# Optimization experiments

Measured on AMD Instinct MI355X. Metric: run time of the kernel, lower is better.

Reference implementation:

```python
import jax, jax.numpy as jnp
import numpy as np

B, C_LIDAR, C_CAM = 2, 384, 80
H = W = 180
HW = H * W
HID, NCLS, P, NH, DFF, L, NMS_K = 128, 10, 200, 8, 256, 2, 3


def conv2d(x, w, b):
    y = jax.lax.conv_general_dilated(x, w, (1, 1), 'SAME', dimension_numbers=('NCHW', 'OIHW', 'NCHW'))
    return y + b[None, :, None, None]


def conv1d3(x, w, b):
    y = jax.lax.conv_general_dilated(x, w, (1,), 'SAME', dimension_numbers=('NCH', 'OIH', 'NCH'))
    return y + b[None, :, None]


def layer_norm(x, g, b, eps=1e-5):
    mu = jnp.mean(x, -1, keepdims=True)
    var = jnp.mean((x - mu) ** 2, -1, keepdims=True)
    return (x - mu) * jax.lax.rsqrt(var + eps) * g + b


def mha(q, k, v, wqkv, bqkv, wo, bo):
    Bq, Nq, C = q.shape
    dh = C // NH
    qh = (q @ wqkv[0].T + bqkv[0]).reshape(Bq, Nq, NH, dh)
    kh = (k @ wqkv[1].T + bqkv[1]).reshape(k.shape[0], -1, NH, dh)
    vh = (v @ wqkv[2].T + bqkv[2]).reshape(v.shape[0], -1, NH, dh)
    att = jax.nn.softmax(jnp.einsum('bqhd,bkhd->bhqk', qh, kh) * np.float32(1.0 / np.sqrt(dh)), axis=-1)
    out = jnp.einsum('bhqk,bkhd->bqhd', att, vh).reshape(Bq, Nq, C)
    return out @ wo.T + bo


def posembed(pos, w1, b1, g, bt, w2, b2):
    # Conv1d(2->C,k1) + BN(inference) + ReLU + Conv1d(C->C,k1); pos [B,N,2] -> [B,N,C]
    x = pos @ w1.T + b1
    x = jax.nn.relu(x * g + bt)
    return x @ w2.T + b2


def reference(lidar, cam, shared_w, shared_b, fused_w, fused_b, hm_w1, hm_b1, hm_g, hm_beta, hm_w2, hm_b2, ce_w, ce_b, pe_w1, pe_b1, pe_g, pe_beta, pe_w2, pe_b2, attn_wqkv, attn_bqkv, attn_wo, attn_bo, ln_g, ln_b, ffn_w1, ffn_b1, ffn_w2, ffn_b2, hc_w1, hc_b1, hc_g, hc_beta, hc_w2, hc_b2, hh_w1, hh_b1, hh_g, hh_beta, hh_w2, hh_b2):
    cam_feat = conv2d(cam, fused_w, fused_b)            # [B,HID,H,W]
    lidar_feat = conv2d(lidar, shared_w, shared_b)      # [B,HID,H,W]
    lidar_flat = lidar_feat.reshape(B, HID, HW)
    key_flat = cam_feat.reshape(B, HID, HW).transpose(0, 2, 1)   # [B,HW,HID]
    # heatmap head: ConvModule(conv+BN+ReLU) then conv -> classes
    h = jax.nn.relu(conv2d(lidar_feat, hm_w1, hm_b1) * hm_g[None, :, None, None] + hm_beta[None, :, None, None])
    dense_heatmap = conv2d(h, hm_w2, hm_b2)             # [B,NCLS,H,W]
    heatmap = jax.nn.sigmoid(jax.lax.stop_gradient(dense_heatmap))
    # max-pool local-max NMS
    pad = NMS_K // 2
    inner = jax.lax.reduce_window(heatmap, -jnp.inf, jax.lax.max, (1, 1, NMS_K, NMS_K), (1, 1, 1, 1), 'VALID')
    local_max = jnp.zeros_like(heatmap).at[:, :, pad:-pad, pad:-pad].set(inner)
    # nuScenes: classes 8,9 use kernel-size-1 pooling (identity)
    local_max = local_max.at[:, 8].set(heatmap[:, 8]).at[:, 9].set(heatmap[:, 9])
    heatmap = heatmap * (heatmap == local_max)
    # top-k proposals over flattened class*HW scores (== descending argsort[:P])
    _, top = jax.lax.top_k(heatmap.reshape(B, -1), P)
    top_cls = top // HW
    top_idx = top % HW
    qf = jnp.take_along_axis(lidar_flat, top_idx[:, None, :], axis=2)   # [B,HID,P]
    one_hot = jax.nn.one_hot(top_cls, NCLS, dtype=qf.dtype)             # [B,P,NCLS]
    qf = qf + (one_hot @ ce_w.T + ce_b).transpose(0, 2, 1)
    # BEV position grid (x/y cell centers, ij order matching HW flattening)
    gx = jnp.arange(H, dtype=qf.dtype) + 0.5
    gy = jnp.arange(W, dtype=qf.dtype) + 0.5
    bev = jnp.stack(jnp.meshgrid(gx, gy, indexing='ij'), -1).reshape(HW, 2)
    qpos = bev[top_idx]                                  # [B,P,2]
    x = qf.transpose(0, 2, 1)                            # [B,P,HID]
    for i in range(L):
        qpe = posembed(qpos, pe_w1[i, 0], pe_b1[i, 0], pe_g[i, 0], pe_beta[i, 0], pe_w2[i, 0], pe_b2[i, 0])
        kpe = posembed(bev[None], pe_w1[i, 1], pe_b1[i, 1], pe_g[i, 1], pe_beta[i, 1], pe_w2[i, 1], pe_b2[i, 1])
        k = key_flat + kpe
        sa = mha(x + qpe, x + qpe, x + qpe, attn_wqkv[i, 0], attn_bqkv[i, 0], attn_wo[i, 0], attn_bo[i, 0])
        x = layer_norm(x + sa, ln_g[i, 0], ln_b[i, 0])
        ca = mha(x + qpe, k, k, attn_wqkv[i, 1], attn_bqkv[i, 1], attn_wo[i, 1], attn_bo[i, 1])
        x = layer_norm(x + ca, ln_g[i, 1], ln_b[i, 1])
        f = jax.nn.relu(x @ ffn_w1[i].T + ffn_b1[i]) @ ffn_w2[i].T + ffn_b2[i]
        x = layer_norm(x + f, ln_g[i, 2], ln_b[i, 2])
        xc = x.transpose(0, 2, 1)                        # [B,HID,P]
        yc = jax.nn.relu(conv1d3(xc, hc_w1[i], hc_b1[i]) * hc_g[i][None, :, None] + hc_beta[i][None, :, None])
        center = conv1d3(yc, hc_w2[i], hc_b2[i]) + qpos.transpose(0, 2, 1)
        yh = jax.nn.relu(conv1d3(xc, hh_w1[i], hh_b1[i]) * hh_g[i][None, :, None] + hh_beta[i][None, :, None])
        hm_pred = conv1d3(yh, hh_w2[i], hh_b2[i])
        qpos = jax.lax.stop_gradient(center).transpose(0, 2, 1)   # .detach().clone().permute
    return jnp.concatenate([center, hm_pred], axis=1)   # [B, 2+NCLS, P]


def _n(key, i, shape, s=0.02):
    return s * jax.random.normal(jax.random.fold_in(key, i), shape, dtype=jnp.float32)


def setup_inputs():
    key = jax.random.key(0)
    z, o = jnp.zeros, jnp.ones
    return dict(
        lidar=jax.random.normal(jax.random.fold_in(key, 100), (B, C_LIDAR, H, W), dtype=jnp.float32),
        cam=jax.random.normal(jax.random.fold_in(key, 101), (B, C_CAM, H, W), dtype=jnp.float32),
        shared_w=_n(key, 0, (HID, C_LIDAR, 3, 3)), shared_b=z((HID,)),
        fused_w=_n(key, 1, (HID, C_CAM, 3, 3)), fused_b=z((HID,)),
        hm_w1=_n(key, 2, (HID, HID, 3, 3)), hm_b1=z((HID,)), hm_g=o((HID,)), hm_beta=z((HID,)),
        hm_w2=_n(key, 3, (NCLS, HID, 3, 3)), hm_b2=z((NCLS,)),
        ce_w=_n(key, 4, (HID, NCLS)), ce_b=z((HID,)),
        pe_w1=_n(key, 5, (L, 2, HID, 2), 0.1), pe_b1=z((L, 2, HID)),
        pe_g=o((L, 2, HID)), pe_beta=z((L, 2, HID)),
        pe_w2=_n(key, 6, (L, 2, HID, HID)), pe_b2=z((L, 2, HID)),
        attn_wqkv=_n(key, 7, (L, 2, 3, HID, HID), 0.05), attn_bqkv=z((L, 2, 3, HID)),
        attn_wo=_n(key, 8, (L, 2, HID, HID), 0.05), attn_bo=z((L, 2, HID)),
        ln_g=o((L, 3, HID)), ln_b=z((L, 3, HID)),
        ffn_w1=_n(key, 9, (L, DFF, HID)), ffn_b1=z((L, DFF)),
        ffn_w2=_n(key, 10, (L, HID, DFF)), ffn_b2=z((L, HID)),
        hc_w1=_n(key, 11, (L, HID, HID, 3)), hc_b1=z((L, HID)), hc_g=o((L, HID)), hc_beta=z((L, HID)),
        hc_w2=_n(key, 12, (L, 2, HID, 3)), hc_b2=z((L, 2)),
        hh_w1=_n(key, 13, (L, HID, HID, 3)), hh_b1=z((L, HID)), hh_g=o((L, HID)), hh_beta=z((L, HID)),
        hh_w2=_n(key, 14, (L, NCLS, HID, 3)), hh_b2=z((L, NCLS)),
    )
```

## Files before the change

### kernel.cpp

```cpp
#include <hip/hip_runtime.h>
#include <hip/hip_bf16.h>

typedef __hip_bfloat16 bf16;
typedef _Float16 f16;

#define HW 32400
#define NCLS 10
#define PQ 200
#define HIDDEN 128
#define NSPLIT 45
#define SPLITLEN 720
#define CHK 32
#define CAP 6144
#define NBIN 4096
#define L2E 1.44269504f

typedef __attribute__((ext_vector_type(8))) _Float16 half8;
typedef __attribute__((ext_vector_type(8))) short short8;
typedef __attribute__((ext_vector_type(4))) short short4v;
typedef __attribute__((ext_vector_type(4))) float f32x4;

__device__ __forceinline__ float b2f(bf16 v) { return __bfloat162float(v); }
__device__ __forceinline__ void stf(float* p, float v) { *p = v; }
__device__ __forceinline__ void stf(bf16* p, float v) { *p = __float2bfloat16(v); }
__device__ __forceinline__ float ldsel(const void* p, long i, unsigned isbf) {
  return isbf ? __bfloat162float(((const bf16*)p)[i]) : ((const float*)p)[i];
}
__device__ __forceinline__ float ldf(const float* p, long i) { return p[i]; }
__device__ __forceinline__ float ldf(const bf16* p, long i) { return __bfloat162float(p[i]); }
__device__ __forceinline__ short f2bf_bits(float v) {
  union { bf16 h; short s; } u; u.h = __float2bfloat16(v); return u.s;
}
__device__ __forceinline__ short f2h_bits(float v) {
  union { f16 h; short s; } u; u.h = (f16)v; return u.s;
}

__global__ void detect_k(const unsigned* __restrict__ L, unsigned* __restrict__ FLAGS)
{
  __shared__ unsigned cnt[2];
  int tid = threadIdx.x;
  if (tid < 2) cnt[tid] = 0;
  __syncthreads();
  unsigned nz = 0, pl = 0;
  for (int w = tid; w < 4096; w += 256) {
    unsigned u = L[w];
    if (u) {
      nz++;
      unsigned e = (u >> 7) & 0xFF;
      if (e >= 110 && e <= 140) pl++;
    }
  }
  atomicAdd(&cnt[0], nz);
  atomicAdd(&cnt[1], pl);
  __syncthreads();
  if (tid == 0) {
    FLAGS[0] = (2u * cnt[1] > cnt[0]) ? 1u : 0u;
    FLAGS[1] = 0u;
  }
}

struct CvtArgs { const void* src[40]; int n[40]; int off[40]; };
__global__ __launch_bounds__(256) void cvt_k(CvtArgs a, float* __restrict__ dst,
                                             const unsigned* __restrict__ FLAGS)
{
  int j = blockIdx.y;
  unsigned isbf = FLAGS[0];
  int n = a.n[j];
  const void* s = a.src[j];
  float* d = dst + a.off[j];
  for (int t = blockIdx.x * 256 + threadIdx.x; t < n; t += gridDim.x * 256)
    d[t] = ldsel(s, t, isbf);
}

__global__ __launch_bounds__(256) void wprep_k(const float* __restrict__ Wsrc,
    short* __restrict__ WB, int N, int K, int KB, int NTG, int split,
    const unsigned* __restrict__ FLAGS, int dynmode)
{
  unsigned isbf = dynmode ? FLAGS[0] : 0u;
  long total = (long)(split ? 2 : 1) * 9 * KB * NTG * 512;
  for (long t = (long)blockIdx.x * 256 + threadIdx.x; t < total;
       t += (long)gridDim.x * 256) {
    long r = t;
    int k = (int)(r & 31); r >>= 5;
    int n16 = (int)(r & 15); r >>= 4;
    int nt = (int)(r % NTG); r /= NTG;
    int kb = (int)(r % KB); r /= KB;
    int tap = (int)(r % 9); r /= 9;
    int plane = (int)r;
    int n = nt * 16 + n16, kk = kb * 32 + k;
    float v = 0.f;
    if (n < N && kk < K) v = Wsrc[((long)n * K + kk) * 9 + tap];
    short outv;
    if (isbf) {
      outv = (plane == 0) ? f2bf_bits(v) : (short)0;
    } else {
      f16 h = (f16)v;
      if (plane == 0) outv = f2h_bits((float)h);
      else outv = f2h_bits((v - (float)h) * 4096.0f);
    }
    WB[t] = outv;
  }
}

template <int MODE, int WM, int WN, int MT, int NT, int CW, typename CT>
__global__ __launch_bounds__(256) void conv_mfma(
    const void* __restrict__ A, const unsigned* __restrict__ FLAGS, int dyn,
    int gate, long abatch,
    const short* __restrict__ WB, const float* __restrict__ bias,
    const float* __restrict__ g, const float* __restrict__ beta, int act,
    CT* __restrict__ C, long cbatch, int N, int K, int KB, int NTG)
{
  constexpr int CPR = 180 / CW;
  constexpr int TOT = 180 * CPR;
  constexpr int BAND = (TOT + 7) / 8;
  constexpr int PXS = WM * MT * 16 + 2;
  constexpr int AW = 3 * PXS * 40;
  __shared__ __align__(16) short Ah[AW];
  __shared__ __align__(16) short Al[MODE == 3 ? AW : 8];
  if (gate >= 0 && FLAGS[0] != (unsigned)gate) return;
  int gsw = blockIdx.x;
  int idx = (gsw & 7) * BAND + (gsw >> 3);
  if (idx >= TOT) return;
  unsigned isbf = dyn ? FLAGS[0] : 0u;
  int bz = blockIdx.z;
  int y = idx / CPR;
  int x0 = (idx % CPR) * CW;
  int tid = threadIdx.x;
  int w = tid >> 6, lane = tid & 63;
  int lane15 = lane & 15, lgrp = lane >> 4;
  int wm = w % WM, wn = w / WM;
  int mbase = wm * MT * 16;
  int nbase = wn * NT * 16;
  f32x4 accM[MT][NT] = {};
  f32x4 accC[MODE == 3 ? MT : 1][MODE == 3 ? NT : 1] = {};
  long planeStride = (long)9 * KB * NTG * 512;

  for (int kb = 0; kb < KB; kb++) {
    __syncthreads();
    for (int u = tid; u < 3 * PXS * 4; u += 256) {
      int px = u % PXS;
      int t2 = u / PXS;
      int kg = t2 & 3, row = t2 >> 2;
      int gx = x0 + px - 1, gy = y + row - 1;
      bool in = (gx >= 0 && gx < 180 && gy >= 0 && gy < 180);
      long gbase = (long)bz * abatch + (long)(kb * 32 + kg * 8) * HW +
                   (long)gy * 180 + gx;
      short8 hv, lv;
#pragma unroll
      for (int j = 0; j < 8; j++) {
        int kk = kb * 32 + kg * 8 + j;
        if constexpr (MODE == 1) {
          hv[j] = (in && kk < K) ? ((const short*)A)[gbase + (long)j * HW]
                                 : (short)0;
        } else {
          float v = (in && kk < K) ? ldsel(A, gbase + (long)j * HW, isbf) : 0.f;
          f16 h = (f16)v;
          hv[j] = f2h_bits((float)h);
          if constexpr (MODE == 3) lv[j] = f2h_bits((v - (float)h) * 4096.0f);
        }
      }
      int o = (row * PXS + px) * 40 + kg * 8;
      *(short8*)&Ah[o] = hv;
      if constexpr (MODE == 3) *(short8*)&Al[o] = lv;
    }
    __syncthreads();
#pragma unroll
    for (int tap = 0; tap < 9; tap++) {
      int ty = tap / 3, tx = tap % 3;
      const short* wb = WB + (((long)tap * KB + kb) * NTG) * 512;
      if constexpr (MODE == 1) {
        short8 bh[NT];
#pragma unroll
        for (int nt = 0; nt < NT; nt++) {
          long o = (long)(wn * NT + nt) * 512 + lane15 * 32 + lgrp * 8;
          bh[nt] = *(const short8*)(wb + o);
        }
        short8 ah[MT];
#pragma unroll
        for (int mt = 0; mt < MT; mt++) {
          int px = mbase + mt * 16 + lane15 + tx;
          ah[mt] = *(const short8*)&Ah[(ty * PXS + px) * 40 + lgrp * 8];
        }
#pragma unroll
        for (int mt = 0; mt < MT; mt++)
#pragma unroll
          for (int nt = 0; nt < NT; nt++)
            accM[mt][nt] = __builtin_amdgcn_mfma_f32_16x16x32_bf16(
                ah[mt], bh[nt], accM[mt][nt], 0, 0, 0);
      } else {
        half8 bh[NT], bl[MODE == 3 ? NT : 1];
#pragma unroll
        for (int nt = 0; nt < NT; nt++) {
          long o = (long)(wn * NT + nt) * 512 + lane15 * 32 + lgrp * 8;
          bh[nt] = *(const half8*)(wb + o);
          if constexpr (MODE == 3) bl[nt] = *(const half8*)(wb + planeStride + o);
        }
        half8 ah[MT], al[MODE == 3 ? MT : 1];
#pragma unroll
        for (int mt = 0; mt < MT; mt++) {
          int px = mbase + mt * 16 + lane15 + tx;
          int o = (ty * PXS + px) * 40 + lgrp * 8;
          ah[mt] = *(const half8*)&Ah[o];
          if constexpr (MODE == 3) al[mt] = *(const half8*)&Al[o];
        }
#pragma unroll
        for (int mt = 0; mt < MT; mt++)
#pragma unroll
          for (int nt = 0; nt < NT; nt++) {
            accM[mt][nt] = __builtin_amdgcn_mfma_f32_16x16x32_f16(
                ah[mt], bh[nt], accM[mt][nt], 0, 0, 0);
            if constexpr (MODE == 3) {
              accC[mt][nt] = __builtin_amdgcn_mfma_f32_16x16x32_f16(
                  al[mt], bh[nt], accC[mt][nt], 0, 0, 0);
              accC[mt][nt] = __builtin_amdgcn_mfma_f32_16x16x32_f16(
                  ah[mt], bl[nt], accC[mt][nt], 0, 0, 0);
            }
          }
      }
    }
  }
  int pixbase = y * 180 + x0;
#pragma unroll
  for (int mt = 0; mt < MT; mt++) {
    int m = mbase + mt * 16 + lgrp * 4;
    if (m >= CW) continue;
#pragma unroll
    for (int nt = 0; nt < NT; nt++) {
      int n = nbase + nt * 16 + lane15;
      if (n >= N) continue;
      float bi = bias[n];
      float gg = g ? g[n] : 1.f;
      float bb = g ? beta[n] : 0.f;
      long base = (long)bz * cbatch + (long)n * HW + pixbase + m;
      float vv[4];
#pragma unroll
      for (int r = 0; r < 4; r++) {
        float v = accM[mt][nt][r];
        if constexpr (MODE == 3) v += accC[mt][nt][r] * (1.f / 4096.f);
        v += bi;
        if (g) v = v * gg + bb;
        if (act == 1) v = fmaxf(v, 0.f);
        else if (act == 2) v = 1.f / (1.f + expf(-v));
        vv[r] = v;
      }
      if constexpr (sizeof(CT) == 4) {
        if (m + 3 < CW) {
          f32x4 ov; ov[0] = vv[0]; ov[1] = vv[1]; ov[2] = vv[2]; ov[3] = vv[3];
          *(f32x4*)&C[base] = ov;
        } else {
#pragma unroll
          for (int r = 0; r < 4; r++) if (m + r < CW) C[base + r] = vv[r];
        }
      } else {
        if (m + 3 < CW) {
          short4v ov;
#pragma unroll
          for (int r = 0; r < 4; r++) ov[r] = f2bf_bits(vv[r]);
          *(short4v*)&C[base] = ov;
        } else {
#pragma unroll
          for (int r = 0; r < 4; r++)
            if (m + r < CW) *((short*)&C[base + r]) = f2bf_bits(vv[r]);
        }
      }
    }
  }
}

__global__ __launch_bounds__(256) void kvproj_k(
    const bf16* __restrict__ A1, const bf16* __restrict__ A2,
    const float* __restrict__ Wf, const float* __restrict__ bias,
    bf16* __restrict__ C)
{
  __shared__ __align__(16) short As[64 * 40];
  int m0 = blockIdx.x * 64;
  int n0 = blockIdx.y * 64;
  int b = blockIdx.z;
  int tid = threadIdx.x;
  int w = tid >> 6, lane = tid & 63;
  int lane15 = lane & 15, lgrp = lane >> 4;
  int wm = w & 1, wn = w >> 1;
  const bf16* A1b = A1 + (long)b * 128 * HW;
  f32x4 acc[2][2] = {};
  for (int kb = 0; kb < 4; kb++) {
    __syncthreads();
    for (int e = tid; e < 2048; e += 256) {
      int k = e >> 6, m = e & 63;
      int gm = m0 + m;
      float v = 0.f;
      if (gm < HW) {
        long idx = (long)(kb * 32 + k) * HW + gm;
        v = b2f(A1b[idx]) + b2f(A2[idx]);
      }
      As[m * 40 + k] = f2bf_bits(v);
    }
    __syncthreads();
    short8 bh[2];
#pragma unroll
    for (int nt = 0; nt < 2; nt++) {
      int n = n0 + wn * 32 + nt * 16 + lane15;
      const float* wr = Wf + (long)n * 128 + kb * 32 + lgrp * 8;
      float4 w0 = *(const float4*)wr;
      float4 w1 = *(const float4*)(wr + 4);
      short8 t;
      t[0] = f2bf_bits(w0.x); t[1] = f2bf_bits(w0.y);
      t[2] = f2bf_bits(w0.z); t[3] = f2bf_bits(w0.w);
      t[4] = f2bf_bits(w1.x); t[5] = f2bf_bits(w1.y);
      t[6] = f2bf_bits(w1.z); t[7] = f2bf_bits(w1.w);
      bh[nt] = t;
    }
    short8 ah[2];
#pragma unroll
    for (int mt = 0; mt < 2; mt++) {
      int m = wm * 32 + mt * 16 + lane15;
      ah[mt] = *(const short8*)&As[m * 40 + lgrp * 8];
    }
#pragma unroll
    for (int mt = 0; mt < 2; mt++)
#pragma unroll
      for (int nt = 0; nt < 2; nt++)
        acc[mt][nt] = __builtin_amdgcn_mfma_f32_16x16x32_bf16(
            ah[mt], bh[nt], acc[mt][nt], 0, 0, 0);
  }
#pragma unroll
  for (int mt = 0; mt < 2; mt++) {
    int mq = m0 + wm * 32 + mt * 16 + lgrp * 4;
    if (mq >= HW) continue;
#pragma unroll
    for (int nt = 0; nt < 2; nt++) {
      int n = n0 + wn * 32 + nt * 16 + lane15;
      float bi = bias[n];
      short4v ov;
#pragma unroll
      for (int r = 0; r < 4; r++) ov[r] = f2bf_bits(acc[mt][nt][r] + bi);
      *(short4v*)&C[(long)b * 256 * HW + (long)n * HW + mq] = ov;
    }
  }
}

template <typename AT, typename CT>
__global__ __launch_bounds__(256) void gemm_k(
    const AT* __restrict__ A, const AT* __restrict__ A2, int lda, int amode,
    long abatch,
    const float* __restrict__ W, const float* __restrict__ bias, int act,
    const float* __restrict__ res,
    const float* __restrict__ pe1w, const float* __restrict__ pe1b,
    const float* __restrict__ pe1g, const float* __restrict__ pe1bt,
    CT* __restrict__ C, int ldc, int cmode, long cbatch,
    int M, int N, int K)
{
  __shared__ __align__(16) float As[16][68];
  __shared__ __align__(16) float Ws[16][68];
  int b = blockIdx.z;
  int m0 = blockIdx.x * 64, n0 = blockIdx.y * 64;
  int tid = threadIdx.x;
  int nt = tid & 15, mt = tid >> 4;
  float acc[4][4] = {};
  const AT* Ab = A + (long)b * abatch;
  for (int k0 = 0; k0 < K; k0 += 16) {
    if (amode == 0) {
      for (int e = tid; e < 1024; e += 256) {
        int m = e >> 4, k = e & 15;
        float v = 0.f;
        if (m0 + m < M) {
          long idx = (long)(m0 + m) * lda + k0 + k;
          v = ldf(Ab, idx);
          if (A2) v += ldf(A2, idx);
        }
        As[k][m] = v;
      }
    } else if (amode == 2) {
      for (int e = tid; e < 1024; e += 256) {
        int m = e & 63, k = e >> 6;
        float v = 0.f;
        int gm = m0 + m;
        if (gm < M) {
          float p0 = (float)(gm / 180) + 0.5f;
          float p1 = (float)(gm % 180) + 0.5f;
          int kk = k0 + k;
          float t = p0 * pe1w[kk * 2] + p1 * pe1w[kk * 2 + 1] + pe1b[kk];
          t = t * pe1g[kk] + pe1bt[kk];
          v = fmaxf(t, 0.f);
        }
        As[k][m] = v;
      }
    } else {
      const float* qp = (const float*)A;
      for (int e = tid; e < 1024; e += 256) {
        int m = e & 63, k = e >> 6;
        float v = 0.f;
        int gm = m0 + m;
        if (gm < M) {
          float p0 = qp[gm * 2], p1 = qp[gm * 2 + 1];
          int kk = k0 + k;
          float t = p0 * pe1w[kk * 2] + p1 * pe1w[kk * 2 + 1] + pe1b[kk];
          t = t * pe1g[kk] + pe1bt[kk];
          v = fmaxf(t, 0.f);
        }
        As[k][m] = v;
      }
    }
    for (int e = tid; e < 1024; e += 256) {
      int n = e >> 4, k = e & 15;
      float v = 0.f;
      if (n0 + n < N) v = W[(long)(n0 + n) * K + k0 + k];
      Ws[k][n] = v;
    }
    __syncthreads();
#pragma unroll
    for (int kk = 0; kk < 16; kk++) {
      float4 av = *(const float4*)&As[kk][mt * 4];
      float4 wv = *(const float4*)&Ws[kk][nt * 4];
      float am[4] = {av.x, av.y, av.z, av.w};
      float wn[4] = {wv.x, wv.y, wv.z, wv.w};
#pragma unroll
      for (int mi = 0; mi < 4; mi++)
#pragma unroll
        for (int ni = 0; ni < 4; ni++)
          acc[mi][ni] = fmaf(am[mi], wn[ni], acc[mi][ni]);
    }
    __syncthreads();
  }
#pragma unroll
  for (int mi = 0; mi < 4; mi++) {
    int m = m0 + mt * 4 + mi;
    if (m >= M) continue;
#pragma unroll
    for (int ni = 0; ni < 4; ni++) {
      int n = n0 + nt * 4 + ni;
      if (n >= N) continue;
      float v = acc[mi][ni];
      if (bias) v += bias[n];
      if (act == 1) v = fmaxf(v, 0.f);
      if (res) v += res[(long)m * ldc + n];
      long ci = (cmode == 0) ? ((long)b * cbatch + (long)m * ldc + n)
                             : ((long)b * cbatch + (long)n * ldc + m);
      stf(&C[ci], v);
    }
  }
}

__global__ void nms_k(const float* __restrict__ HEAT, float* __restrict__ SCORE)
{
  int t = blockIdx.x * 256 + threadIdx.x;
  if (t >= 2 * NCLS * HW) return;
  int b = t / (NCLS * HW); int r = t % (NCLS * HW);
  int cls = r / HW; int n = r % HW;
  const float* hb = HEAT + ((long)(b * NCLS + cls)) * HW;
  float v = hb[n];
  bool keep = true;
  if (cls < 8) {
    int y = n / 180, x = n % 180;
    if (y == 0 || y == 179 || x == 0 || x == 179) keep = false;
    else {
      float mx = -1e30f;
#pragma unroll
      for (int dy = -1; dy <= 1; dy++)
#pragma unroll
        for (int dx = -1; dx <= 1; dx++)
          mx = fmaxf(mx, hb[(y + dy) * 180 + x + dx]);
      keep = (v == mx);
    }
  }
  SCORE[(long)b * (NCLS * HW) + r] = keep ? v : 0.f;
}

__global__ void zero_u32(unsigned* p, int n)
{
  int t = blockIdx.x * 256 + threadIdx.x;
  if (t < n) p[t] = 0;
}

__global__ __launch_bounds__(256) void hist_k(const float* __restrict__ SCORE,
                                              unsigned* __restrict__ HIST)
{
  __shared__ unsigned lh[NBIN];
  int b = blockIdx.y;
  for (int e = threadIdx.x; e < NBIN; e += 256) lh[e] = 0;
  __syncthreads();
  int start = blockIdx.x * 1350;
  const float* sb = SCORE + (long)b * (NCLS * HW);
  for (int e = start + threadIdx.x; e < start + 1350; e += 256) {
    unsigned bits = __float_as_uint(sb[e]);
    atomicAdd(&lh[bits >> 18], 1u);
  }
  __syncthreads();
  for (int e = threadIdx.x; e < NBIN; e += 256) {
    unsigned c = lh[e];
    if (c) atomicAdd(&HIST[b * NBIN + e], c);
  }
}

__global__ void thresh_k(const unsigned* __restrict__ HIST, unsigned* __restrict__ THR)
{
  __shared__ unsigned ps[256];
  int b = blockIdx.x;
  const unsigned* hb = HIST + b * NBIN;
  unsigned s = 0;
  for (int j = 0; j < 16; j++) s += hb[threadIdx.x * 16 + j];
  ps[threadIdx.x] = s;
  __syncthreads();
  if (threadIdx.x == 0) {
    unsigned cum = 0; int t = 255;
    for (; t > 0; t--) { if (cum + ps[t] >= PQ) break; cum += ps[t]; }
    int bin = t * 16 + 15;
    for (; bin > t * 16; bin--) { unsigned c = hb[bin]; if (cum + c >= PQ) break; cum += c; }
    if (bin < 1) bin = 1;
    THR[b] = (unsigned)bin;
  }
}

__global__ void collect_k(const float* __restrict__ SCORE, const unsigned* __restrict__ THR,
                          unsigned* __restrict__ ACNT, unsigned long long* __restrict__ CAND)
{
  int t = blockIdx.x * 256 + threadIdx.x;
  if (t >= 2 * NCLS * HW) return;
  int b = t / (NCLS * HW); int r = t % (NCLS * HW);
  float v = SCORE[(long)b * (NCLS * HW) + r];
  unsigned bits = __float_as_uint(v);
  if ((bits >> 18) >= THR[b]) {
    unsigned slot = atomicAdd(&ACNT[b], 1u);
    if (slot < CAP) CAND[(long)b * CAP + slot] =
        ((unsigned long long)bits << 32) | (unsigned)(~r);
  }
}

__global__ __launch_bounds__(64) void select_k(
    const unsigned long long* __restrict__ CAND, const unsigned* __restrict__ ACNT,
    unsigned* __restrict__ TOPC, unsigned* __restrict__ TOPI, float* __restrict__ QPA)
{
  __shared__ unsigned long long cnd[CAP];
  int b = blockIdx.x;
  int lane = threadIdx.x;
  unsigned cnt = ACNT[b]; if (cnt > CAP) cnt = CAP;
  for (int e = lane; e < (int)cnt; e += 64) cnd[e] = CAND[(long)b * CAP + e];
  __syncthreads();
  for (int p = 0; p < PQ; p++) {
    unsigned long long best = 0;
    for (int e = lane; e < (int)cnt; e += 64) { unsigned long long c = cnd[e]; if (c > best) best = c; }
#pragma unroll
    for (int o = 32; o; o >>= 1) {
      unsigned long long other = __shfl_xor(best, o, 64);
      if (other > best) best = other;
    }
    for (int e = lane; e < (int)cnt; e += 64) if (best != 0 && cnd[e] == best) cnd[e] = 0;
    if (lane == 0) {
      unsigned idx = (best == 0) ? 0u : ~(unsigned)(best & 0xFFFFFFFFull);
      if (idx >= NCLS * HW) idx = 0;
      unsigned cls = idx / HW, n = idx % HW;
      TOPC[b * PQ + p] = cls; TOPI[b * PQ + p] = n;
      QPA[((long)(b * PQ + p)) * 2 + 0] = (float)(n / 180) + 0.5f;
      QPA[((long)(b * PQ + p)) * 2 + 1] = (float)(n % 180) + 0.5f;
    }
    __syncthreads();
  }
}

__global__ void gather_k(const float* __restrict__ LIDF, const unsigned* __restrict__ TOPC,
                         const unsigned* __restrict__ TOPI, const float* __restrict__ cew,
                         const float* __restrict__ ceb, float* __restrict__ X)
{
  int t = blockIdx.x * 256 + threadIdx.x;
  if (t >= 2 * PQ * HIDDEN) return;
  int c = t & 127; int r = t >> 7; int p = r % PQ; int b = r / PQ;
  unsigned n = TOPI[b * PQ + p]; unsigned cls = TOPC[b * PQ + p];
  if (n >= HW) n = 0;
  if (cls >= NCLS) cls = 0;
  X[t] = LIDF[((long)(b * HIDDEN + c)) * HW + n] + cew[c * NCLS + cls] + ceb[c];
}

__global__ __launch_bounds__(64) void self_attn_k(const float* __restrict__ SQKV,
                                                  float* __restrict__ SAO)
{
  int q = blockIdx.x, h = blockIdx.y, b = blockIdx.z;
  int lane = threadIdx.x;
  const float* qp = SQKV + ((long)(b * PQ + q)) * 384 + h * 16;
  float qv[16];
#pragma unroll
  for (int d = 0; d < 16; d++) qv[d] = qp[d] * 0.25f;
  float sv[4]; int kks[4]; int nk = 0;
  float lmax = -1e30f;
  for (int kk = lane; kk < PQ; kk += 64) {
    const float* kp = SQKV + ((long)(b * PQ + kk)) * 384 + 128 + h * 16;
    float s = 0.f;
#pragma unroll
    for (int d = 0; d < 16; d++) s = fmaf(qv[d], kp[d], s);
    sv[nk] = s; kks[nk] = kk; nk++;
    lmax = fmaxf(lmax, s);
  }
#pragma unroll
  for (int o = 32; o; o >>= 1) lmax = fmaxf(lmax, __shfl_xor(lmax, o, 64));
  float lsum = 0.f; float acc[16] = {};
  for (int t = 0; t < nk; t++) {
    float p = expf(sv[t] - lmax);
    lsum += p;
    const float* vp = SQKV + ((long)(b * PQ + kks[t])) * 384 + 256 + h * 16;
#pragma unroll
    for (int d = 0; d < 16; d++) acc[d] = fmaf(p, vp[d], acc[d]);
  }
#pragma unroll
  for (int o = 32; o; o >>= 1) lsum += __shfl_xor(lsum, o, 64);
#pragma unroll
  for (int d = 0; d < 16; d++) {
    float v = acc[d];
#pragma unroll
    for (int o = 32; o; o >>= 1) v += __shfl_xor(v, o, 64);
    if (lane == 0) SAO[((long)(b * PQ + q)) * HIDDEN + h * 16 + d] = v / lsum;
  }
}

__global__ __launch_bounds__(256) void flash_mfma_k(const float* __restrict__ QH,
                                                    const bf16* __restrict__ KVT,
                                                    float* __restrict__ PART)
{
  __shared__ __align__(16) short Qs[64 * 40];
  __shared__ __align__(16) short Ks[2][32 * 40];
  __shared__ __align__(16) short Vs[2][16 * 40];
  __shared__ __align__(16) short Ps[4][16 * 40];
  int s = blockIdx.x, h = blockIdx.y;
  int b = blockIdx.z >> 2, qb = blockIdx.z & 3;
  int tid = threadIdx.x;
  int w = tid >> 6, lane = tid & 63;
  int lane15 = lane & 15, lgrp = lane >> 4;
  const short* Kb = (const short*)KVT + ((long)b * 256 + h * 16) * HW;
  const short* Vb = Kb + (long)128 * HW;
  int nbeg = s * SPLITLEN;

  for (int e = tid; e < 2 * 32 * 16; e += 256) {
    int buf = e >> 9, rr = e & 511;
    int kk = rr >> 4, d2 = rr & 15;
    Ks[buf][kk * 40 + 16 + d2] = 0;
  }
  {
    int q = tid >> 2, dg = tid & 3;
    int gq = qb * 64 + q;
    short8 v = {};
    if (dg < 2 && gq < PQ) {
      const float* qp = QH + ((long)(b * PQ + gq)) * HIDDEN + h * 16 + dg * 8;
#pragma unroll
      for (int j = 0; j < 8; j++) v[j] = f2bf_bits(qp[j] * 0.25f);
    }
    *(short8*)&Qs[q * 40 + dg * 8] = v;
  }

  auto stageKV = [&](int t, int buf) {
    int kb0 = nbeg + t * CHK;
    for (int e = tid; e < 512; e += 256) {
      int d = e >> 5, kk = e & 31;
      long gk = kb0 + kk; if (gk >= HW) gk = HW - 1;
      long go = (long)d * HW + gk;
      Ks[buf][kk * 40 + d] = Kb[go];
      Vs[buf][d * 40 + kk] = Vb[go];
    }
  };

  stageKV(0, 0);
  __syncthreads();

  short8 aq = *(const short8*)&Qs[(w * 16 + lane15) * 40 + lgrp * 8];
  float m[4] = {-1e30f, -1e30f, -1e30f, -1e30f};
  float l[4] = {0.f, 0.f, 0.f, 0.f};
  f32x4 accO = {};
  const int NTL = (SPLITLEN + CHK - 1) / CHK;
  for (int t = 0; t < NTL; t++) {
    int cur = t & 1;
    if (t + 1 < NTL) stageKV(t + 1, cur ^ 1);
    int valid = SPLITLEN - t * CHK; if (valid > CHK) valid = CHK;
    short8 bk0 = *(const short8*)&Ks[cur][lane15 * 40 + lgrp * 8];
    short8 bk1 = *(const short8*)&Ks[cur][(16 + lane15) * 40 + lgrp * 8];
    f32x4 z = {};
    f32x4 s0 = __builtin_amdgcn_mfma_f32_16x16x32_bf16(aq, bk0, z, 0, 0, 0);
    f32x4 s1 = __builtin_amdgcn_mfma_f32_16x16x32_bf16(aq, bk1, z, 0, 0, 0);
    bool msk0 = (lane15 >= valid);
    bool msk1 = (16 + lane15 >= valid);
#pragma unroll
    for (int r = 0; r < 4; r++) {
      float x0 = msk0 ? -1e30f : s0[r];
      float x1 = msk1 ? -1e30f : s1[r];
      float mx = fmaxf(x0, x1);
      mx = fmaxf(mx, __shfl_xor(mx, 1, 64));
      mx = fmaxf(mx, __shfl_xor(mx, 2, 64));
      mx = fmaxf(mx, __shfl_xor(mx, 4, 64));
      mx = fmaxf(mx, __shfl_xor(mx, 8, 64));
      float mn = fmaxf(m[r], mx);
      float p0 = exp2f((x0 - mn) * L2E);
      float p1 = exp2f((x1 - mn) * L2E);
      float sum = p0 + p1;
      sum += __shfl_xor(sum, 1, 64);
      sum += __shfl_xor(sum, 2, 64);
      sum += __shfl_xor(sum, 4, 64);
      sum += __shfl_xor(sum, 8, 64);
      float al = exp2f((m[r] - mn) * L2E);
      l[r] = l[r] * al + sum;
      m[r] = mn;
      accO[r] *= al;
      Ps[w][(lgrp * 4 + r) * 40 + lane15] = f2bf_bits(p0);
      Ps[w][(lgrp * 4 + r) * 40 + 16 + lane15] = f2bf_bits(p1);
    }
    short8 ap = *(const short8*)&Ps[w][lane15 * 40 + lgrp * 8];
    short8 bv = *(const short8*)&Vs[cur][lane15 * 40 + lgrp * 8];
    accO = __builtin_amdgcn_mfma_f32_16x16x32_bf16(ap, bv, accO, 0, 0, 0);
    __syncthreads();
  }
  long base = ((((long)(b * 8 + h)) * NSPLIT + s) * PQ) * 18;
#pragma unroll
  for (int r = 0; r < 4; r++) {
    int gq = qb * 64 + w * 16 + lgrp * 4 + r;
    if (gq < PQ) {
      long ro = base + (long)gq * 18;
      PART[ro + lane15] = accO[r];
      if (lane15 == 0) { PART[ro + 16] = m[r]; PART[ro + 17] = l[r]; }
    }
  }
}

__global__ void combine_k(const float* __restrict__ PART, float* __restrict__ CAO)
{
  int t = blockIdx.x * 256 + threadIdx.x;
  if (t >= 2 * 8 * PQ * 16) return;
  int d = t & 15; int r = t >> 4;
  int q = r % PQ; r /= PQ;
  int h = r & 7; int b = r >> 3;
  long base = (((long)(b * 8 + h)) * NSPLIT) * PQ * 18 + (long)q * 18;
  float M = -1e30f;
  for (int s = 0; s < NSPLIT; s++) M = fmaxf(M, PART[base + (long)s * PQ * 18 + 16]);
  float L = 0.f, O = 0.f;
  for (int s = 0; s < NSPLIT; s++) {
    long p0 = base + (long)s * PQ * 18;
    float w = expf(PART[p0 + 16] - M);
    L += PART[p0 + 17] * w;
    O += PART[p0 + d] * w;
  }
  CAO[((long)(b * PQ + q)) * HIDDEN + h * 16 + d] = (L > 0.f) ? O / L : 0.f;
}

__global__ __launch_bounds__(256) void ln_k(const float* __restrict__ PRE,
                                            const float* __restrict__ g,
                                            const float* __restrict__ bta,
                                            float* __restrict__ X)
{
  int row = blockIdx.x * 4 + (threadIdx.x >> 6);
  int lane = threadIdx.x & 63;
  const float* p = PRE + (long)row * HIDDEN;
  float v0 = p[lane], v1 = p[lane + 64];
  float s = v0 + v1;
#pragma unroll
  for (int o = 32; o; o >>= 1) s += __shfl_xor(s, o, 64);
  float mu = s * (1.f / 128.f);
  float d0 = v0 - mu, d1 = v1 - mu;
  float vs = d0 * d0 + d1 * d1;
#pragma unroll
  for (int o = 32; o; o >>= 1) vs += __shfl_xor(vs, o, 64);
  float rs = rsqrtf(vs * (1.f / 128.f) + 1e-5f);
  float* xo = X + (long)row * HIDDEN;
  xo[lane] = d0 * rs * g[lane] + bta[lane];
  xo[lane + 64] = d1 * rs * g[lane + 64] + bta[lane + 64];
}

__global__ __launch_bounds__(128) void conv1d_k(const float* __restrict__ X,
                                                const float* __restrict__ w,
                                                const float* __restrict__ bias,
                                                const float* __restrict__ g,
                                                const float* __restrict__ beta,
                                                float* __restrict__ Y)
{
  int p = blockIdx.x, b = blockIdx.y;
  int co = threadIdx.x;
  __shared__ float xs[3][HIDDEN];
  for (int e = co; e < 3 * HIDDEN; e += HIDDEN) {
    int t = e >> 7, c = e & 127;
    int pp = p + t - 1;
    xs[t][c] = (pp >= 0 && pp < PQ) ? X[((long)(b * PQ + pp)) * HIDDEN + c] : 0.f;
  }
  __syncthreads();
  const float* wr = w + (long)co * HIDDEN * 3;
  float acc = 0.f;
  for (int c = 0; c < HIDDEN; c++) {
    acc = fmaf(xs[0][c], wr[c * 3 + 0], acc);
    acc = fmaf(xs[1][c], wr[c * 3 + 1], acc);
    acc = fmaf(xs[2][c], wr[c * 3 + 2], acc);
  }
  float v = (acc + bias[co]) * g[co] + beta[co];
  Y[((long)(b * PQ + p)) * HIDDEN + co] = fmaxf(v, 0.f);
}

__global__ void head2_k(const float* __restrict__ Y, const float* __restrict__ w,
                        const float* __restrict__ bias, const float* __restrict__ qpos,
                        float* __restrict__ OUT, int N, float* __restrict__ qnext)
{
  int t = blockIdx.x * 256 + threadIdx.x;
  if (t >= 2 * N * PQ) return;
  int p = t % PQ; int r = t / PQ; int co = r % N; int b = r / N;
  const float* wr = w + (long)co * HIDDEN * 3;
  float acc = 0.f;
  for (int tap = 0; tap < 3; tap++) {
    int pp = p + tap - 1;
    if (pp < 0 || pp >= PQ) continue;
    const float* yr = Y + ((long)(b * PQ + pp)) * HIDDEN;
    for (int c = 0; c < HIDDEN; c++)
      acc = fmaf(yr[c], wr[c * 3 + tap], acc);
  }
  float v = acc + bias[co];
  if (qpos) v += qpos[((long)(b * PQ + p)) * 2 + co];
  OUT[((long)(b * N + co)) * PQ + p] = v;
  if (qnext) qnext[((long)(b * PQ + p)) * 2 + co] = v;
}

__global__ void out_k(const float* __restrict__ CENT, const float* __restrict__ HMP,
                      void* __restrict__ out, const unsigned* __restrict__ FLAGS)
{
  int t = blockIdx.x * 256 + threadIdx.x;
  if (t >= 2 * 12 * PQ) return;
  int p = t % PQ; int r = t / PQ; int ch = r % 12; int b = r / 12;
  float v = (ch < 2) ? CENT[((long)(b * 2 + ch)) * PQ + p]
                     : HMP[((long)(b * 10 + ch - 2)) * PQ + p];
  if (FLAGS[0]) ((bf16*)out)[t] = __float2bfloat16(v);
  else          ((float*)out)[t] = v;
}

extern "C" void kernel_launch(void* const* d_in, const int* in_sizes, int n_in,
                              void* d_out, int out_size, void* d_ws, size_t ws_size,
                              hipStream_t stream)
{
  (void)n_in; (void)out_size; (void)ws_size;

  float* F = (float*)d_ws;
  size_t off = 0;
  int aoff[42];
  {
    size_t acc = 0;
    for (int i = 2; i < 42; i++) { aoff[i] = (int)acc; acc += (size_t)in_sizes[i]; }
    off = acc;
  }
  float* ARENA = F;
  float* LIDF = F + off;
  bf16*  KVT16 = (bf16*)(F + off);
  off += 8294400;
  float* HBUF = F + off;
  bf16*  KPET16 = (bf16*)(F + off);
  float* PART  = F + off;
  off += 4147200;
  bf16*  CAMF16 = (bf16*)(F + off);
  off += 4147200;
  float* HEAT  = F + off;
  float* SCORE = F + off + 648000;
  off += 1296000;
  float* X   = F + off; off += 51200;
  float* XQ  = F + off; off += 51200;
  float* QPE = F + off; off += 51200;
  float* T1Q = F + off; off += 51200;
  float* SQKV = F + off; off += 153600;
  float* SAO = F + off; off += 51200;
  float* PRE = F + off; off += 51200;
  float* QH2 = F + off; off += 51200;
  float* CAO = F + off; off += 51200;
  float* FF1 = F + off; off += 102400;
  float* YC  = F + off; off += 51200;
  float* CENT = F + off; off += 800;
  float* HMP = F + off; off += 4000;
  float* QPA = F + off; off += 800;
  float* QPB = F + off; off += 800;
  unsigned* U = (unsigned*)(F + off);
  unsigned* HIST  = U;
  unsigned* ACNT  = U + 8192;
  unsigned* THR   = U + 8194;
  unsigned* FLAGS = U + 8196;
  unsigned* TOPC  = U + 8198;
  unsigned* TOPI  = U + 8598;
  unsigned long long* CAND = (unsigned long long*)(U + 9000);
  short* WB_LID = (short*)((((uintptr_t)X) + 15) & ~(uintptr_t)15);
  short* WB_CAM = WB_LID + 884736;
  short* WB_HM1 = WB_CAM + 110592;
  short* WB_HM2 = WB_HM1 + 294912;

  auto W = [&](int i) -> const float* { return ARENA + aoff[i]; };

  detect_k<<<1, 256, 0, stream>>>((const unsigned*)d_in[0], FLAGS);
  {
    CvtArgs a;
    for (int i = 2; i < 42; i++) { a.src[i - 2] = d_in[i]; a.n[i - 2] = in_sizes[i]; a.off[i - 2] = aoff[i]; }
    cvt_k<<<dim3(432, 40), 256, 0, stream>>>(a, ARENA, FLAGS);
  }
  wprep_k<<<3456, 256, 0, stream>>>(W(2), WB_LID, 128, 384, 12, 8, 1, FLAGS, 1);
  wprep_k<<<432, 256, 0, stream>>>(W(4), WB_CAM, 128, 80, 3, 8, 0, FLAGS, 1);
  wprep_k<<<1152, 256, 0, stream>>>(W(6), WB_HM1, 128, 128, 4, 8, 1, FLAGS, 0);
  wprep_k<<<144, 256, 0, stream>>>(W(10), WB_HM2, 10, 128, 4, 1, 1, FLAGS, 0);

  auto gemm = [&](const float* A, const float* A2, int lda, const float* Wp,
                  const float* bias, int act, const float* res, float* C, int ldc,
                  int M, int N, int K) {
    dim3 grid((M + 63) / 64, (N + 63) / 64, 1);
    gemm_k<float, float><<<grid, 256, 0, stream>>>(
        A, A2, lda, 0, 0L, Wp, bias, act, res,
        nullptr, nullptr, nullptr, nullptr, C, ldc, 0, 0L, M, N, K);
  };

  conv_mfma<1, 1, 4, 2, 2, 30, float><<<dim3(1080, 1, 2), 256, 0, stream>>>(
      d_in[0], FLAGS, 1, 1, (long)384 * HW, WB_LID, W(3), nullptr, nullptr, 0,
      LIDF, (long)128 * HW, 128, 384, 12, 8);
  conv_mfma<3, 1, 4, 2, 2, 30, float><<<dim3(1080, 1, 2), 256, 0, stream>>>(
      d_in[0], FLAGS, 1, 0, (long)384 * HW, WB_LID, W(3), nullptr, nullptr, 0,
      LIDF, (long)128 * HW, 128, 384, 12, 8);
  conv_mfma<1, 1, 4, 2, 2, 30, bf16><<<dim3(1080, 1, 2), 256, 0, stream>>>(
      d_in[1], FLAGS, 1, 1, (long)80 * HW, WB_CAM, W(5), nullptr, nullptr, 0,
      CAMF16, (long)128 * HW, 128, 80, 3, 8);
  conv_mfma<0, 1, 4, 2, 2, 30, bf16><<<dim3(1080, 1, 2), 256, 0, stream>>>(
      d_in[1], FLAGS, 1, 0, (long)80 * HW, WB_CAM, W(5), nullptr, nullptr, 0,
      CAMF16, (long)128 * HW, 128, 80, 3, 8);
  for (int b = 0; b < 2; b++) {
    conv_mfma<3, 1, 4, 2, 2, 30, float><<<dim3(1080, 1, 1), 256, 0, stream>>>(
        LIDF + (long)b * 128 * HW, FLAGS, 0, -1, 0L, WB_HM1, W(7), W(8), W(9), 1,
        HBUF, 0L, 128, 128, 4, 8);
    conv_mfma<3, 4, 1, 1, 1, 60, float><<<dim3(544, 1, 1), 256, 0, stream>>>(
        HBUF, FLAGS, 0, -1, 0L, WB_HM2, W(11), nullptr, nullptr, 2,
        HEAT + (long)b * NCLS * HW, 0L, 10, 128, 4, 1);
  }

  nms_k<<<(2 * NCLS * HW + 255) / 256, 256, 0, stream>>>(HEAT, SCORE);
  zero_u32<<<(8196 + 255) / 256, 256, 0, stream>>>(U, 8196);
  hist_k<<<dim3(240, 2), 256, 0, stream>>>(SCORE, HIST);
  thresh_k<<<2, 256, 0, stream>>>(HIST, THR);
  collect_k<<<(2 * NCLS * HW + 255) / 256, 256, 0, stream>>>(SCORE, THR, ACNT, CAND);
  select_k<<<2, 64, 0, stream>>>(CAND, ACNT, TOPC, TOPI, QPA);
  gather_k<<<200, 256, 0, stream>>>(LIDF, TOPC, TOPI, W(12), W(13), X);

  for (int i = 0; i < 2; i++) {
    const float* qcur = (i == 0) ? QPA : QPB;
    float* qnext = (i == 0) ? QPB : QPA;
    gemm_k<float, float><<<dim3(7, 2, 1), 256, 0, stream>>>(
        qcur, (const float*)nullptr, 0, 3, 0L,
        W(18) + (size_t)(i * 2 + 0) * 16384, W(19) + (i * 2 + 0) * 128, 0, nullptr,
        W(14) + (i * 2 + 0) * 256, W(15) + (i * 2 + 0) * 128,
        W(16) + (i * 2 + 0) * 128, W(17) + (i * 2 + 0) * 128,
        QPE, 128, 0, 0L, 400, 128, 128);
    gemm_k<float, bf16><<<dim3(507, 2, 1), 256, 0, stream>>>(
        ARENA, (const float*)nullptr, 0, 2, 0L,
        W(18) + (size_t)(i * 2 + 1) * 16384, W(19) + (i * 2 + 1) * 128, 0, nullptr,
        W(14) + (i * 2 + 1) * 256, W(15) + (i * 2 + 1) * 128,
        W(16) + (i * 2 + 1) * 128, W(17) + (i * 2 + 1) * 128,
        KPET16, HW, 1, 0L, 32400, 128, 128);
    gemm(X, QPE, 128, W(20) + (size_t)(i * 2 + 0) * 49152, W(21) + (i * 2 + 0) * 384,
         0, nullptr, SQKV, 384, 400, 384, 128);
    self_attn_k<<<dim3(200, 8, 2), 64, 0, stream>>>(SQKV, SAO);
    gemm(SAO, nullptr, 128, W(22) + (size_t)(i * 2 + 0) * 16384, W(23) + (i * 2 + 0) * 128,
         0, X, PRE, 128, 400, 128, 128);
    ln_k<<<100, 256, 0, stream>>>(PRE, W(24) + (i * 3 + 0) * 128, W(25) + (i * 3 + 0) * 128, X);
    gemm(X, QPE, 128, W(20) + (size_t)(i * 2 + 1) * 49152, W(21) + (i * 2 + 1) * 384,
         0, nullptr, QH2, 128, 400, 128, 128);
    kvproj_k<<<dim3(507, 4, 2), 256, 0, stream>>>(
        CAMF16, KPET16,
        W(20) + (size_t)(i * 2 + 1) * 49152 + 16384,
        W(21) + (i * 2 + 1) * 384 + 128, KVT16);
    flash_mfma_k<<<dim3(NSPLIT, 8, 8), 256, 0, stream>>>(QH2, KVT16, PART);
    combine_k<<<200, 256, 0, stream>>>(PART, CAO);
    gemm(CAO, nullptr, 128, W(22) + (size_t)(i * 2 + 1) * 16384, W(23) + (i * 2 + 1) * 128,
         0, X, PRE, 128, 400, 128, 128);
    ln_k<<<100, 256, 0, stream>>>(PRE, W(24) + (i * 3 + 1) * 128, W(25) + (i * 3 + 1) * 128, X);
    gemm(X, nullptr, 128, W(26) + (size_t)i * 32768, W(27) + i * 256,
         1, nullptr, FF1, 256, 400, 256, 128);
    gemm(FF1, nullptr, 256, W(28) + (size_t)i * 32768, W(29) + i * 128,
         0, X, PRE, 128, 400, 128, 256);
    ln_k<<<100, 256, 0, stream>>>(PRE, W(24) + (i * 3 + 2) * 128, W(25) + (i * 3 + 2) * 128, X);
    conv1d_k<<<dim3(200, 2), 128, 0, stream>>>(X, W(30) + (size_t)i * 49152,
        W(31) + i * 128, W(32) + i * 128, W(33) + i * 128, YC);
    head2_k<<<4, 256, 0, stream>>>(YC, W(34) + (size_t)i * 768, W(35) + i * 2,
        qcur, CENT, 2, qnext);
    conv1d_k<<<dim3(200, 2), 128, 0, stream>>>(X, W(36) + (size_t)i * 49152,
        W(37) + i * 128, W(38) + i * 128, W(39) + i * 128, YC);
    head2_k<<<16, 256, 0, stream>>>(YC, W(40) + (size_t)i * 3840, W(41) + i * 10,
        nullptr, HMP, 10, nullptr);
  }
  out_k<<<19, 256, 0, stream>>>(CENT, HMP, d_out, FLAGS);
}
```

Measured before the change: 2.023 ms.

## Use MFMA for key posembed GEMM, retile convs, batch heatmap convs

Replaces the scalar FP32 tiled GEMM for the key positional-embedding projection with a bf16 MFMA kernel that builds the first-layer ReLU activations directly in shared memory. The input convolutions are retiled to larger 60-wide tiles with half as many blocks. When the workspace is large enough, the heatmap conv pair runs as a single batched launch over both batches using an extra buffer instead of a per-batch loop. This trades FP32 accuracy in the posembed GEMM for tensor-core throughput and adds a workspace-size-dependent code path.

```diff
diff --git a/kernel.cpp b/kernel.cpp
--- a/kernel.cpp
+++ b/kernel.cpp
@@ -338,6 +338,80 @@
   }
 }
 
+__global__ __launch_bounds__(256) void kpe_mfma_k(
+    const float* __restrict__ pe1w, const float* __restrict__ pe1b,
+    const float* __restrict__ pe1g, const float* __restrict__ pe1bt,
+    const float* __restrict__ W2, const float* __restrict__ b2,
+    bf16* __restrict__ C)
+{
+  __shared__ __align__(16) short As[64 * 40];
+  int m0 = blockIdx.x * 64;
+  int n0 = blockIdx.y * 64;
+  int tid = threadIdx.x;
+  int w = tid >> 6, lane = tid & 63;
+  int lane15 = lane & 15, lgrp = lane >> 4;
+  int wm = w & 1, wn = w >> 1;
+  f32x4 acc[2][2] = {};
+  for (int kb = 0; kb < 4; kb++) {
+    __syncthreads();
+    for (int e = tid; e < 2048; e += 256) {
+      int k = e >> 6, m = e & 63;
+      int gm = m0 + m;
+      int kk = kb * 32 + k;
+      float v = 0.f;
+      if (gm < HW) {
+        float p0 = (float)(gm / 180) + 0.5f;
+        float p1 = (float)(gm % 180) + 0.5f;
+        float t = p0 * pe1w[kk * 2] + p1 * pe1w[kk * 2 + 1] + pe1b[kk];
+        t = t * pe1g[kk] + pe1bt[kk];
+        v = fmaxf(t, 0.f);
+      }
+      As[m * 40 + k] = f2bf_bits(v);
+    }
+    __syncthreads();
+    short8 bh[2];
+#pragma unroll
+    for (int nt = 0; nt < 2; nt++) {
+      int n = n0 + wn * 32 + nt * 16 + lane15;
+      const float* wr = W2 + (long)n * 128 + kb * 32 + lgrp * 8;
+      float4 w0 = *(const float4*)wr;
+      float4 w1 = *(const float4*)(wr + 4);
+      short8 t;
+      t[0] = f2bf_bits(w0.x); t[1] = f2bf_bits(w0.y);
+      t[2] = f2bf_bits(w0.z); t[3] = f2bf_bits(w0.w);
+      t[4] = f2bf_bits(w1.x); t[5] = f2bf_bits(w1.y);
+      t[6] = f2bf_bits(w1.z); t[7] = f2bf_bits(w1.w);
+      bh[nt] = t;
+    }
+    short8 ah[2];
+#pragma unroll
+    for (int mt = 0; mt < 2; mt++) {
+      int m = wm * 32 + mt * 16 + lane15;
+      ah[mt] = *(const short8*)&As[m * 40 + lgrp * 8];
+    }
+#pragma unroll
+    for (int mt = 0; mt < 2; mt++)
+#pragma unroll
+      for (int nt = 0; nt < 2; nt++)
+        acc[mt][nt] = __builtin_amdgcn_mfma_f32_16x16x32_bf16(
+            ah[mt], bh[nt], acc[mt][nt], 0, 0, 0);
+  }
+#pragma unroll
+  for (int mt = 0; mt < 2; mt++) {
+    int mq = m0 + wm * 32 + mt * 16 + lgrp * 4;
+    if (mq >= HW) continue;
+#pragma unroll
+    for (int nt = 0; nt < 2; nt++) {
+      int n = n0 + wn * 32 + nt * 16 + lane15;
+      float bi = b2[n];
+      short4v ov;
+#pragma unroll
+      for (int r = 0; r < 4; r++) ov[r] = f2bf_bits(acc[mt][nt][r] + bi);
+      *(short4v*)&C[(long)n * HW + mq] = ov;
+    }
+  }
+}
+
 template <typename AT, typename CT>
 __global__ __launch_bounds__(256) void gemm_k(
     const AT* __restrict__ A, const AT* __restrict__ A2, int lda, int amode,
@@ -366,21 +440,6 @@
           long idx = (long)(m0 + m) * lda + k0 + k;
           v = ldf(Ab, idx);
           if (A2) v += ldf(A2, idx);
-        }
-        As[k][m] = v;
-      }
-    } else if (amode == 2) {
-      for (int e = tid; e < 1024; e += 256) {
-        int m = e & 63, k = e >> 6;
-        float v = 0.f;
-        int gm = m0 + m;
-        if (gm < M) {
-          float p0 = (float)(gm / 180) + 0.5f;
-          float p1 = (float)(gm % 180) + 0.5f;
-          int kk = k0 + k;
-          float t = p0 * pe1w[kk * 2] + p1 * pe1w[kk * 2 + 1] + pe1b[kk];
-          t = t * pe1g[kk] + pe1bt[kk];
-          v = fmaxf(t, 0.f);
         }
         As[k][m] = v;
       }
@@ -822,7 +881,7 @@
                               void* d_out, int out_size, void* d_ws, size_t ws_size,
                               hipStream_t stream)
 {
-  (void)n_in; (void)out_size; (void)ws_size;
+  (void)n_in; (void)out_size;
 
   float* F = (float*)d_ws;
   size_t off = 0;
@@ -868,6 +927,10 @@
   unsigned* TOPC  = U + 8198;
   unsigned* TOPI  = U + 8598;
   unsigned long long* CAND = (unsigned long long*)(U + 9000);
+  size_t end_floats = off + 9000 + 2 * CAP * 2;
+  float* HBUF2 = nullptr;
+  if (ws_size >= (end_floats + 8294400) * sizeof(float))
+    HBUF2 = F + end_floats;
   short* WB_LID = (short*)((((uintptr_t)X) + 15) & ~(uintptr_t)15);
   short* WB_CAM = WB_LID + 884736;
   short* WB_HM1 = WB_CAM + 110592;
@@ -895,25 +958,34 @@
         nullptr, nullptr, nullptr, nullptr, C, ldc, 0, 0L, M, N, K);
   };
 
-  conv_mfma<1, 1, 4, 2, 2, 30, float><<<dim3(1080, 1, 2), 256, 0, stream>>>(
+  conv_mfma<1, 1, 4, 4, 2, 60, float><<<dim3(544, 1, 2), 256, 0, stream>>>(
       d_in[0], FLAGS, 1, 1, (long)384 * HW, WB_LID, W(3), nullptr, nullptr, 0,
       LIDF, (long)128 * HW, 128, 384, 12, 8);
-  conv_mfma<3, 1, 4, 2, 2, 30, float><<<dim3(1080, 1, 2), 256, 0, stream>>>(
+  conv_mfma<3, 1, 4, 4, 2, 60, float><<<dim3(544, 1, 2), 256, 0, stream>>>(
       d_in[0], FLAGS, 1, 0, (long)384 * HW, WB_LID, W(3), nullptr, nullptr, 0,
       LIDF, (long)128 * HW, 128, 384, 12, 8);
-  conv_mfma<1, 1, 4, 2, 2, 30, bf16><<<dim3(1080, 1, 2), 256, 0, stream>>>(
+  conv_mfma<1, 1, 4, 4, 2, 60, bf16><<<dim3(544, 1, 2), 256, 0, stream>>>(
       d_in[1], FLAGS, 1, 1, (long)80 * HW, WB_CAM, W(5), nullptr, nullptr, 0,
       CAMF16, (long)128 * HW, 128, 80, 3, 8);
-  conv_mfma<0, 1, 4, 2, 2, 30, bf16><<<dim3(1080, 1, 2), 256, 0, stream>>>(
+  conv_mfma<0, 1, 4, 4, 2, 60, bf16><<<dim3(544, 1, 2), 256, 0, stream>>>(
       d_in[1], FLAGS, 1, 0, (long)80 * HW, WB_CAM, W(5), nullptr, nullptr, 0,
       CAMF16, (long)128 * HW, 128, 80, 3, 8);
-  for (int b = 0; b < 2; b++) {
-    conv_mfma<3, 1, 4, 2, 2, 30, float><<<dim3(1080, 1, 1), 256, 0, stream>>>(
-        LIDF + (long)b * 128 * HW, FLAGS, 0, -1, 0L, WB_HM1, W(7), W(8), W(9), 1,
-        HBUF, 0L, 128, 128, 4, 8);
-    conv_mfma<3, 4, 1, 1, 1, 60, float><<<dim3(544, 1, 1), 256, 0, stream>>>(
-        HBUF, FLAGS, 0, -1, 0L, WB_HM2, W(11), nullptr, nullptr, 2,
-        HEAT + (long)b * NCLS * HW, 0L, 10, 128, 4, 1);
+  if (HBUF2) {
+    conv_mfma<3, 1, 4, 4, 2, 60, float><<<dim3(544, 1, 2), 256, 0, stream>>>(
+        LIDF, FLAGS, 0, -1, (long)128 * HW, WB_HM1, W(7), W(8), W(9), 1,
+        HBUF2, (long)128 * HW, 128, 128, 4, 8);
+    conv_mfma<3, 4, 1, 1, 1, 60, float><<<dim3(544, 1, 2), 256, 0, stream>>>(
+        HBUF2, FLAGS, 0, -1, (long)128 * HW, WB_HM2, W(11), nullptr, nullptr, 2,
+        HEAT, (long)NCLS * HW, 10, 128, 4, 1);
+  } else {
+    for (int b = 0; b < 2; b++) {
+      conv_mfma<3, 1, 4, 4, 2, 60, float><<<dim3(544, 1, 1), 256, 0, stream>>>(
+          LIDF + (long)b * 128 * HW, FLAGS, 0, -1, 0L, WB_HM1, W(7), W(8), W(9), 1,
+          HBUF, 0L, 128, 128, 4, 8);
+      conv_mfma<3, 4, 1, 1, 1, 60, float><<<dim3(544, 1, 1), 256, 0, stream>>>(
+          HBUF, FLAGS, 0, -1, 0L, WB_HM2, W(11), nullptr, nullptr, 2,
+          HEAT + (long)b * NCLS * HW, 0L, 10, 128, 4, 1);
+    }
   }
 
   nms_k<<<(2 * NCLS * HW + 255) / 256, 256, 0, stream>>>(HEAT, SCORE);
@@ -933,12 +1005,11 @@
         W(14) + (i * 2 + 0) * 256, W(15) + (i * 2 + 0) * 128,
         W(16) + (i * 2 + 0) * 128, W(17) + (i * 2 + 0) * 128,
         QPE, 128, 0, 0L, 400, 128, 128);
-    gemm_k<float, bf16><<<dim3(507, 2, 1), 256, 0, stream>>>(
-        ARENA, (const float*)nullptr, 0, 2, 0L,
-        W(18) + (size_t)(i * 2 + 1) * 16384, W(19) + (i * 2 + 1) * 128, 0, nullptr,
+    kpe_mfma_k<<<dim3(507, 2), 256, 0, stream>>>(
         W(14) + (i * 2 + 1) * 256, W(15) + (i * 2 + 1) * 128,
         W(16) + (i * 2 + 1) * 128, W(17) + (i * 2 + 1) * 128,
-        KPET16, HW, 1, 0L, 32400, 128, 128);
+        W(18) + (size_t)(i * 2 + 1) * 16384, W(19) + (i * 2 + 1) * 128,
+        KPET16);
     gemm(X, QPE, 128, W(20) + (size_t)(i * 2 + 0) * 49152, W(21) + (i * 2 + 0) * 384,
          0, nullptr, SQKV, 384, 400, 384, 128);
     self_attn_k<<<dim3(200, 8, 2), 64, 0, stream>>>(SQKV, SAO);
```

Result: faster. 1.903 ms (-5.9%).
